# Kernel optimization log

Measured on AMD Instinct MI355X. Metric: run time of the kernel, lower is better.

Reference implementation:

```python
import jax, jax.numpy as jnp
import numpy as np

D_MODEL = 1024
NUM_HEADS = 16
HEAD_DIM = D_MODEL // NUM_HEADS
NEG_INF = -1e9


def setup_inputs() -> dict:
    key = jax.random.key(0)
    ks = jax.random.split(key, 9)
    B, S, SI = 4, 1024, 512
    scale = 1.0 / np.sqrt(D_MODEL)
    return {
        "hidden_states": jax.random.normal(ks[0], (B, S, D_MODEL), jnp.float32),
        "image_hidden_states": jax.random.normal(ks[1], (B, SI, D_MODEL), jnp.float32),
        "attention_mask": jax.random.randint(ks[2], (B, 1, S, S + SI), 0, 2, jnp.int32),
        "w_q": jax.random.normal(ks[3], (D_MODEL, D_MODEL), jnp.float32) * scale,
        "w_k": jax.random.normal(ks[4], (D_MODEL, D_MODEL), jnp.float32) * scale,
        "w_v": jax.random.normal(ks[5], (D_MODEL, D_MODEL), jnp.float32) * scale,
        "u_k": jax.random.normal(ks[6], (D_MODEL, D_MODEL), jnp.float32) * scale,
        "u_v": jax.random.normal(ks[7], (D_MODEL, D_MODEL), jnp.float32) * scale,
        "w_o": jax.random.normal(ks[8], (D_MODEL, D_MODEL), jnp.float32) * scale,
    }


def _split_heads(x):
    # [B, S, D] -> [B, H, S, Dh]
    B, S, _ = x.shape
    return x.reshape(B, S, NUM_HEADS, HEAD_DIM).transpose(0, 2, 1, 3)


def reference(hidden_states, image_hidden_states, attention_mask,
              w_q, w_k, w_v, u_k, u_v, w_o):
    # nn.Linear(bias=False): y = x @ W.T
    q = _split_heads(hidden_states @ w_q.T)          # [B,H,S,Dh]
    k = _split_heads(hidden_states @ w_k.T)          # [B,H,S,Dh]
    v = _split_heads(hidden_states @ w_v.T)
    k_img = _split_heads(image_hidden_states @ u_k.T)  # [B,H,SI,Dh]
    v_img = _split_heads(image_hidden_states @ u_v.T)
    k = jnp.concatenate([k, k_img], axis=2)          # [B,H,S+SI,Dh]
    v = jnp.concatenate([v, v_img], axis=2)

    scores = jnp.einsum('bhqd,bhkd->bhqk', q, k) / np.sqrt(HEAD_DIM)
    scores = jnp.where(attention_mask == 0, NEG_INF, scores)
    p_attn = jax.nn.softmax(scores, axis=-1)         # dropout p=0.0 (eval)
    x = jnp.einsum('bhqk,bhkd->bhqd', p_attn, v)     # [B,H,S,Dh]
    B, H, S, Dh = x.shape
    x = x.transpose(0, 2, 1, 3).reshape(B, S, D_MODEL)
    return x @ w_o.T
```

## Files before the change

### kernel.cpp

```cpp
#include <hip/hip_runtime.h>
#include <stdint.h>


typedef unsigned short u16;
typedef short bf16x8v __attribute__((ext_vector_type(8)));
typedef float f32x4 __attribute__((ext_vector_type(4)));

__device__ __forceinline__ u16 f2bf(float f) {
  union { float f; uint32_t u; } x; x.f = f;
  uint32_t r = x.u + 0x7FFFu + ((x.u >> 16) & 1u);
  return (u16)(r >> 16);
}

__device__ __forceinline__ uint32_t cvtpk(float a, float b) {
  uint32_t r;
  asm("v_cvt_pk_bf16_f32 %0, %1, %2" : "=v"(r) : "v"(a), "v"(b));
  return r;
}

__device__ __forceinline__ float maskand(float e, uint32_t msrc, int off) {
  uint32_t mm = (uint32_t)((int32_t)(msrc << (31 - off)) >> 31);
  union { float f; uint32_t u; } x; x.f = e; x.u &= mm; return x.f;
}

__device__ __forceinline__ void gl_lds16(const u16* g, u16* l) {
  __builtin_amdgcn_global_load_lds((const __attribute__((address_space(1))) unsigned int*)g,
                                   (__attribute__((address_space(3))) unsigned int*)l,
                                   16, 0, 0);
}

__global__ __launch_bounds__(256) void mask_pack(const int* __restrict__ mk,
                                                 uint32_t* __restrict__ Mw) {
  int w = blockIdx.x * 256 + threadIdx.x;
  const int4* p = (const int4*)(mk + (size_t)w * 32);
  uint32_t bits = 0;
  #pragma unroll
  for (int c = 0; c < 8; ++c) {
    int4 v = p[c];
    bits |= (uint32_t)(v.x != 0) << (4 * c);
    bits |= (uint32_t)(v.y != 0) << (4 * c + 1);
    bits |= (uint32_t)(v.z != 0) << (4 * c + 2);
    bits |= (uint32_t)(v.w != 0) << (4 * c + 3);
  }
  Mw[w] = bits;
}

__global__ __launch_bounds__(512, 2) void gemm_qkv(
    const float* __restrict__ Hs, const float* __restrict__ Im,
    const float* __restrict__ Wq, const float* __restrict__ Wk, const float* __restrict__ Wv,
    const float* __restrict__ Uk, const float* __restrict__ Uv,
    u16* __restrict__ Qd, u16* __restrict__ Kd, u16* __restrict__ Vd)
{
  __shared__ __align__(16) u16 As[2 * 16384];
  __shared__ __align__(16) u16 Bs[2 * 16384];
  const int hb = blockIdx.x;
  const int xcd = hb & 7, slot = hb >> 3;
  int bid = (slot < 24) ? xcd * 24 + slot : 192 + xcd * 8 + (slot - 24);
  const float *Ap, *Bp;
  int bm, bn, mode;
  if (bid < 192) { mode = 4; bm = (bid / 12) * 256; bn = (bid % 12) * 256;
                   Ap = Hs + (size_t)bm * 1024;
                   Bp = ((bn < 1024) ? Wq : (bn < 2048) ? Wk : Wv) + (size_t)(bn & 1023) * 1024; }
  else           { mode = 5; int r = bid - 192; bm = (r >> 3) * 256; bn = (r & 7) * 256;
                   Ap = Im + (size_t)bm * 1024;
                   Bp = ((bn < 1024) ? Uk : Uv) + (size_t)(bn & 1023) * 1024; }
  const int tid = threadIdx.x, lane = tid & 63, wave = tid >> 6;
  const int wr = wave >> 2, wc = wave & 3;
  const int g = lane >> 4, c = lane & 15, cs = c & 7;
  const int srow = tid >> 3;
  const int pch  = tid & 7;
  const int gsw  = (pch ^ (srow & 7)) * 8;

  f32x4 zf = {0.f, 0.f, 0.f, 0.f};
  f32x4 acc[8][4];
  #pragma unroll
  for (int f = 0; f < 8; ++f)
    #pragma unroll
    for (int nf = 0; nf < 4; ++nf) acc[f][nf] = zf;

  float4 sa[4][2], sb[4][2];

  #define LOAD_A(kt)                                                               \
    _Pragma("unroll")                                                              \
    for (int j_ = 0; j_ < 4; ++j_) {                                               \
      const float* p_ = Ap + (size_t)(j_ * 64 + srow) * 1024 + (kt) * 64 + gsw;    \
      sa[j_][0] = *(const float4*)p_;                                              \
      sa[j_][1] = *(const float4*)(p_ + 4);                                        \
    }
  #define LOAD_B(kt)                                                               \
    _Pragma("unroll")                                                              \
    for (int j_ = 0; j_ < 4; ++j_) {                                               \
      const float* p_ = Bp + (size_t)(j_ * 64 + srow) * 1024 + (kt) * 64 + gsw;    \
      sb[j_][0] = *(const float4*)p_;                                              \
      sb[j_][1] = *(const float4*)(p_ + 4);                                        \
    }
  #define CVT_A(buf)                                                               \
    _Pragma("unroll")                                                              \
    for (int j_ = 0; j_ < 4; ++j_) {                                               \
      uint4 w_;                                                                    \
      w_.x = cvtpk(sa[j_][0].x, sa[j_][0].y);                                      \
      w_.y = cvtpk(sa[j_][0].z, sa[j_][0].w);                                      \
      w_.z = cvtpk(sa[j_][1].x, sa[j_][1].y);                                      \
      w_.w = cvtpk(sa[j_][1].z, sa[j_][1].w);                                      \
      *(uint4*)&As[(buf) + (j_ * 64 + srow) * 64 + pch * 8] = w_;                  \
    }
  #define CVT_B(buf)                                                               \
    _Pragma("unroll")                                                              \
    for (int j_ = 0; j_ < 4; ++j_) {                                               \
      uint4 w_;                                                                    \
      w_.x = cvtpk(sb[j_][0].x, sb[j_][0].y);                                      \
      w_.y = cvtpk(sb[j_][0].z, sb[j_][0].w);                                      \
      w_.z = cvtpk(sb[j_][1].x, sb[j_][1].y);                                      \
      w_.w = cvtpk(sb[j_][1].z, sb[j_][1].w);                                      \
      *(uint4*)&Bs[(buf) + (j_ * 64 + srow) * 64 + pch * 8] = w_;                  \
    }

  LOAD_A(0); LOAD_B(0);
  CVT_A(0);  CVT_B(0);
  __syncthreads();

  for (int kt = 0; kt < 16; ++kt) {
    const int bc = (kt & 1) * 16384;
    const int bx = bc ^ 16384;
    if (kt < 15) LOAD_A(kt + 1);

    bf16x8v Bf[4][2];
    #pragma unroll
    for (int nf = 0; nf < 4; ++nf)
      #pragma unroll
      for (int ks = 0; ks < 2; ++ks)
        Bf[nf][ks] = *(const bf16x8v*)&Bs[bc + (wc * 64 + nf * 16 + c) * 64 + ((ks * 4 + g) ^ cs) * 8];

    #pragma unroll
    for (int p = 0; p < 4; ++p) {
      bf16x8v Af[2][2];
      #pragma unroll
      for (int i = 0; i < 2; ++i)
        #pragma unroll
        for (int ks = 0; ks < 2; ++ks)
          Af[i][ks] = *(const bf16x8v*)&As[bc + (wr * 128 + (p * 2 + i) * 16 + c) * 64 + ((ks * 4 + g) ^ cs) * 8];
      __builtin_amdgcn_s_setprio(1);
      #pragma unroll
      for (int i = 0; i < 2; ++i)
        #pragma unroll
        for (int nf = 0; nf < 4; ++nf)
          #pragma unroll
          for (int ks = 0; ks < 2; ++ks)
            acc[p * 2 + i][nf] =
              __builtin_amdgcn_mfma_f32_16x16x32_bf16(Af[i][ks], Bf[nf][ks], acc[p * 2 + i][nf], 0, 0, 0);
      __builtin_amdgcn_s_setprio(0);
      if (p == 1 && kt < 15) {
        __builtin_amdgcn_sched_barrier(0);
        CVT_A(bx);
        LOAD_B(kt + 1);
        __builtin_amdgcn_sched_barrier(0);
      }
    }
    if (kt < 15) {
      __builtin_amdgcn_sched_barrier(0);
      CVT_B(bx);
    }
    __syncthreads();
  }
  #undef LOAD_A
  #undef LOAD_B
  #undef CVT_A
  #undef CVT_B

  #pragma unroll
  for (int f = 0; f < 8; ++f) {
    #pragma unroll
    for (int nf = 0; nf < 4; ++nf) {
      #pragma unroll
      for (int j = 0; j < 4; ++j) {
        int gm = bm + wr * 128 + f * 16 + 4 * g + j;
        int gn = bn + wc * 64 + nf * 16 + c;
        float v = acc[f][nf][j];
        if (mode == 4) {
          int b_ = gm >> 10, s_ = gm & 1023;
          if (gn < 1024)      Qd[(size_t)gm * 1024 + gn] = f2bf(v * 0.18033688011112042f);
          else if (gn < 2048) Kd[(size_t)(b_ * 1536 + s_) * 1024 + (gn - 1024)] = f2bf(v);
          else                Vd[(size_t)(b_ * 1024 + (gn - 2048)) * 1536 + s_] = f2bf(v);
        } else {
          int b_ = gm >> 9, s_ = gm & 511;
          if (gn < 1024) Kd[(size_t)(b_ * 1536 + 1024 + s_) * 1024 + gn] = f2bf(v);
          else           Vd[(size_t)(b_ * 1024 + (gn - 1024)) * 1536 + 1024 + s_] = f2bf(v);
        }
      }
    }
  }
}

__global__ __launch_bounds__(256) void gemm_out(const u16* __restrict__ A, const float* __restrict__ Bw,
                                                float* __restrict__ Cout)
{
  __shared__ __align__(16) u16 As2[2 * 8192];
  __shared__ __align__(16) u16 Bs2[2 * 8192];
  const int hb = blockIdx.x;
  const int xcd = hb & 7, slot = hb >> 3;
  const int rg = xcd * 4 + (slot >> 3);
  const int cg = slot & 7;
  const int bm = rg * 128, bn = cg * 128;
  const int tid  = threadIdx.x;
  const int lane = tid & 63, wave = tid >> 6;
  const int wr = wave >> 1, wc = wave & 1;
  const int g = lane >> 4, c = lane & 15, cs = c & 7;
  const int sr  = tid >> 3;
  const int pch = tid & 7;
  const int gsw = (pch ^ (sr & 7)) * 8;

  f32x4 zf = {0.f, 0.f, 0.f, 0.f};
  f32x4 acc[4][4];
  #pragma unroll
  for (int mi = 0; mi < 4; ++mi)
    #pragma unroll
    for (int ni = 0; ni < 4; ++ni) acc[mi][ni] = zf;

  float4 sb[4][2];

  #define STG_A(buf, kt)                                                           \
    _Pragma("unroll")                                                              \
    for (int q_ = 0; q_ < 4; ++q_) {                                               \
      int row_ = q_ * 32 + sr;                                                     \
      gl_lds16(A + (size_t)(bm + row_) * 1024 + (kt) * 64 + gsw,                   \
               &As2[(buf) + row_ * 64 + pch * 8]);                                 \
    }
  #define LOAD_B(kt)                                                               \
    _Pragma("unroll")                                                              \
    for (int q_ = 0; q_ < 4; ++q_) {                                               \
      const float* p_ = Bw + (size_t)(bn + q_ * 32 + sr) * 1024 + (kt) * 64 + gsw; \
      sb[q_][0] = *(const float4*)p_;                                              \
      sb[q_][1] = *(const float4*)(p_ + 4);                                        \
    }
  #define CVT_B(buf)                                                               \
    _Pragma("unroll")                                                              \
    for (int q_ = 0; q_ < 4; ++q_) {                                               \
      uint4 w_;                                                                    \
      w_.x = cvtpk(sb[q_][0].x, sb[q_][0].y);                                      \
      w_.y = cvtpk(sb[q_][0].z, sb[q_][0].w);                                      \
      w_.z = cvtpk(sb[q_][1].x, sb[q_][1].y);                                      \
      w_.w = cvtpk(sb[q_][1].z, sb[q_][1].w);                                      \
      *(uint4*)&Bs2[(buf) + (q_ * 32 + sr) * 64 + pch * 8] = w_;                   \
    }

  STG_A(0, 0);
  LOAD_B(0);
  CVT_B(0);
  __syncthreads();

  for (int kt = 0; kt < 16; ++kt) {
    const int bc = (kt & 1) * 8192;
    const int bx = bc ^ 8192;
    if (kt < 15) { STG_A(bx, kt + 1); LOAD_B(kt + 1); }

    #pragma unroll
    for (int ks = 0; ks < 2; ++ks) {
      bf16x8v af[4], bfr[4];
      #pragma unroll
      for (int mi = 0; mi < 4; ++mi)
        af[mi] = *(const bf16x8v*)&As2[bc + (wr * 64 + mi * 16 + c) * 64 + ((ks * 4 + g) ^ cs) * 8];
      #pragma unroll
      for (int ni = 0; ni < 4; ++ni)
        bfr[ni] = *(const bf16x8v*)&Bs2[bc + (wc * 64 + ni * 16 + c) * 64 + ((ks * 4 + g) ^ cs) * 8];
      __builtin_amdgcn_s_setprio(1);
      #pragma unroll
      for (int mi = 0; mi < 4; ++mi)
        #pragma unroll
        for (int ni = 0; ni < 4; ++ni)
          acc[mi][ni] = __builtin_amdgcn_mfma_f32_16x16x32_bf16(af[mi], bfr[ni], acc[mi][ni], 0, 0, 0);
      __builtin_amdgcn_s_setprio(0);
    }
    if (kt < 15) {
      __builtin_amdgcn_sched_barrier(0);
      CVT_B(bx);
    }
    __syncthreads();
  }
  #undef STG_A
  #undef LOAD_B
  #undef CVT_B

  #pragma unroll
  for (int mi = 0; mi < 4; ++mi)
    #pragma unroll
    for (int ni = 0; ni < 4; ++ni)
      #pragma unroll
      for (int j = 0; j < 4; ++j) {
        int gm = bm + wr * 64 + mi * 16 + 4 * g + j;
        int gn = bn + wc * 64 + ni * 16 + c;
        Cout[(size_t)gm * 1024 + gn] = acc[mi][ni][j];
      }
}

__global__ __launch_bounds__(256) void attn_kernel(const u16* __restrict__ Q, const u16* __restrict__ Kc,
                                                   const u16* __restrict__ Vt,
                                                   const uint32_t* __restrict__ Mw,
                                                   u16* __restrict__ AO)
{
  const int bid = blockIdx.x;
  const int grp = bid & 63;
  const int qt  = bid >> 6;
  const int h = grp & 15, b = grp >> 4;
  const int q0 = qt * 64;
  const int tid = threadIdx.x, lane = tid & 63, wave = tid >> 6;
  const int g = lane >> 4, c = lane & 15;
  const int qw = q0 + wave * 16;

  __shared__ __align__(16) u16 Ks[64 * 64];
  __shared__ __align__(16) u16 Vs[64 * 64];
  __shared__ __align__(16) u16 Ps[4][16 * 72];

  bf16x8v qf0, qf1;
  {
    const u16* qp = Q + (size_t)(b * 1024 + qw + c) * 1024 + h * 64 + g * 8;
    qf0 = *(const bf16x8v*)qp;
    qf1 = *(const bf16x8v*)(qp + 32);
  }
  f32x4 zf = {0.f, 0.f, 0.f, 0.f};
  f32x4 O[4];
  float l = 0.f;
  #pragma unroll
  for (int dt = 0; dt < 4; ++dt) O[dt] = zf;

  const int sr  = tid >> 3;
  const int pch = tid & 7;
  const int swz = (pch ^ (sr & 7)) * 8;
  const int cs  = c & 7;
  const u16* Kbase = Kc + (size_t)(b * 1536) * 1024 + h * 64;
  const u16* Vbase = Vt + (size_t)(b * 1024 + h * 64) * 1536;
  const uint32_t* mrow = Mw + (size_t)(b * 1024 + qw + c) * 48;

  bf16x8v kr0, kr1, vr0, vr1;
  kr0 = *(const bf16x8v*)(Kbase + (size_t)sr * 1024 + pch * 8);
  kr1 = *(const bf16x8v*)(Kbase + (size_t)(32 + sr) * 1024 + pch * 8);
  vr0 = *(const bf16x8v*)(Vbase + (size_t)sr * 1536 + pch * 8);
  vr1 = *(const bf16x8v*)(Vbase + (size_t)(32 + sr) * 1536 + pch * 8);
  *(bf16x8v*)&Ks[sr * 64 + swz]        = kr0;
  *(bf16x8v*)&Ks[(32 + sr) * 64 + swz] = kr1;
  *(bf16x8v*)&Vs[sr * 64 + swz]        = vr0;
  *(bf16x8v*)&Vs[(32 + sr) * 64 + swz] = vr1;
  __syncthreads();

  for (int kt = 0; kt < 24; ++kt) {
    if (kt < 23) {
      const int ln = (kt + 1) * 64;
      kr0 = *(const bf16x8v*)(Kbase + (size_t)(ln + sr) * 1024 + pch * 8);
      kr1 = *(const bf16x8v*)(Kbase + (size_t)(ln + 32 + sr) * 1024 + pch * 8);
      vr0 = *(const bf16x8v*)(Vbase + (size_t)sr * 1536 + ln + pch * 8);
      vr1 = *(const bf16x8v*)(Vbase + (size_t)(32 + sr) * 1536 + ln + pch * 8);
    }
    uint2 mwv = *(const uint2*)(mrow + kt * 2);

    f32x4 s[4];
    __builtin_amdgcn_s_setprio(1);
    #pragma unroll
    for (int nt = 0; nt < 4; ++nt) {
      const u16* kr = &Ks[(nt * 16 + c) * 64];
      bf16x8v k0 = *(const bf16x8v*)&kr[(g ^ cs) * 8];
      bf16x8v k1 = *(const bf16x8v*)&kr[((4 + g) ^ cs) * 8];
      f32x4 z = zf;
      z = __builtin_amdgcn_mfma_f32_16x16x32_bf16(k0, qf0, z, 0, 0, 0);
      z = __builtin_amdgcn_mfma_f32_16x16x32_bf16(k1, qf1, z, 0, 0, 0);
      s[nt] = z;
    }
    __builtin_amdgcn_s_setprio(0);

    uint64_t mq = (((uint64_t)mwv.y << 32) | (uint64_t)mwv.x) >> (4 * g);
    uint32_t mlo = (uint32_t)mq, mhi = (uint32_t)(mq >> 32);
    #pragma unroll
    for (int nt = 0; nt < 4; ++nt) {
      uint32_t msrc = (nt < 2) ? mlo : mhi;
      #pragma unroll
      for (int j = 0; j < 4; ++j) {
        float e = exp2f(s[nt][j]);
        float p = maskand(e, msrc, 16 * (nt & 1) + j);
        s[nt][j] = p;
        l += p;
      }
    }

    u16* pw = &Ps[wave][0];
    #pragma unroll
    for (int nt = 0; nt < 4; ++nt) {
      uint2 pk2;
      pk2.x = cvtpk(s[nt][0], s[nt][1]);
      pk2.y = cvtpk(s[nt][2], s[nt][3]);
      *(uint2*)&pw[c * 72 + nt * 16 + g * 4] = pk2;
    }
    bf16x8v pb0 = *(const bf16x8v*)&pw[c * 72 + g * 8];
    bf16x8v pb1 = *(const bf16x8v*)&pw[c * 72 + 32 + g * 8];
    __builtin_amdgcn_s_setprio(1);
    #pragma unroll
    for (int dt = 0; dt < 4; ++dt) {
      const u16* vr = &Vs[(dt * 16 + c) * 64];
      bf16x8v v0 = *(const bf16x8v*)&vr[(g ^ cs) * 8];
      bf16x8v v1 = *(const bf16x8v*)&vr[((4 + g) ^ cs) * 8];
      O[dt] = __builtin_amdgcn_mfma_f32_16x16x32_bf16(v0, pb0, O[dt], 0, 0, 0);
      O[dt] = __builtin_amdgcn_mfma_f32_16x16x32_bf16(v1, pb1, O[dt], 0, 0, 0);
    }
    __builtin_amdgcn_s_setprio(0);

    __syncthreads();
    if (kt < 23) {
      *(bf16x8v*)&Ks[sr * 64 + swz]        = kr0;
      *(bf16x8v*)&Ks[(32 + sr) * 64 + swz] = kr1;
      *(bf16x8v*)&Vs[sr * 64 + swz]        = vr0;
      *(bf16x8v*)&Vs[(32 + sr) * 64 + swz] = vr1;
      __syncthreads();
    }
  }

  float r = l;
  r += __shfl_xor(r, 16);
  r += __shfl_xor(r, 32);
  float inv = 1.f / r;
  size_t ro = (size_t)(b * 1024 + qw + c) * 1024 + h * 64;
  #pragma unroll
  for (int dt = 0; dt < 4; ++dt) {
    uint2 st;
    st.x = cvtpk(O[dt][0] * inv, O[dt][1] * inv);
    st.y = cvtpk(O[dt][2] * inv, O[dt][3] * inv);
    *(uint2*)&AO[ro + dt * 16 + 4 * g] = st;
  }
}

extern "C" void kernel_launch(void* const* d_in, const int* in_sizes, int n_in,
                              void* d_out, int out_size, void* d_ws, size_t ws_size,
                              hipStream_t stream) {
  (void)in_sizes; (void)n_in; (void)out_size; (void)ws_size;
  const float* hs = (const float*)d_in[0];
  const float* im = (const float*)d_in[1];
  const int*   mk = (const int*)d_in[2];
  const float* wq = (const float*)d_in[3];
  const float* wk = (const float*)d_in[4];
  const float* wv = (const float*)d_in[5];
  const float* uk = (const float*)d_in[6];
  const float* uv = (const float*)d_in[7];
  const float* wo = (const float*)d_in[8];

  char* ws = (char*)d_ws;
  u16* Qb  = (u16*)(ws + 0);
  u16* Kb  = (u16*)(ws + 8388608);
  u16* Vtb = (u16*)(ws + 20971520);
  u16* AO  = (u16*)(ws + 33554432);
  uint32_t* Mw = (uint32_t*)(ws + 41943040);

  mask_pack<<<768, 256, 0, stream>>>(mk, Mw);
  gemm_qkv<<<256, 512, 0, stream>>>(hs, im, wq, wk, wv, uk, uv, Qb, Kb, Vtb);
  attn_kernel<<<1024, 256, 0, stream>>>(Qb, Kb, Vtb, Mw, AO);
  gemm_out<<<256, 256, 0, stream>>>(AO, wo, (float*)d_out);
}
```

Baseline: 158.9 us.

## Fuse mask bit-packing into QKV GEMM prologue and vectorize V-transpose stores

Removes the separate mask_pack launch and has each QKV GEMM thread pack mask words right after issuing its first tile loads. This saves one kernel launch and lets the mask read overlap with the GEMM's own loads. The epilogue is also split by output region so the branch on gn moves out of the inner loops, and the transposed V writes become packed 8-byte bf16 stores instead of scalar ones. The catch is that the GEMM prologue gets longer, since the ~25MB mask read now sits on the GEMM's critical path and may raise register pressure.

Result: faster. 133.7 us (-15.9%).

```diff
diff --git a/kernel.cpp b/kernel.cpp
--- a/kernel.cpp
+++ b/kernel.cpp
@@ -29,27 +29,13 @@
                                    16, 0, 0);
 }
 
-__global__ __launch_bounds__(256) void mask_pack(const int* __restrict__ mk,
-                                                 uint32_t* __restrict__ Mw) {
-  int w = blockIdx.x * 256 + threadIdx.x;
-  const int4* p = (const int4*)(mk + (size_t)w * 32);
-  uint32_t bits = 0;
-  #pragma unroll
-  for (int c = 0; c < 8; ++c) {
-    int4 v = p[c];
-    bits |= (uint32_t)(v.x != 0) << (4 * c);
-    bits |= (uint32_t)(v.y != 0) << (4 * c + 1);
-    bits |= (uint32_t)(v.z != 0) << (4 * c + 2);
-    bits |= (uint32_t)(v.w != 0) << (4 * c + 3);
-  }
-  Mw[w] = bits;
-}
-
 __global__ __launch_bounds__(512, 2) void gemm_qkv(
     const float* __restrict__ Hs, const float* __restrict__ Im,
     const float* __restrict__ Wq, const float* __restrict__ Wk, const float* __restrict__ Wv,
     const float* __restrict__ Uk, const float* __restrict__ Uv,
-    u16* __restrict__ Qd, u16* __restrict__ Kd, u16* __restrict__ Vd)
+    const int* __restrict__ Mk,
+    u16* __restrict__ Qd, u16* __restrict__ Kd, u16* __restrict__ Vd,
+    uint32_t* __restrict__ Mw)
 {
   __shared__ __align__(16) u16 As[2 * 16384];
   __shared__ __align__(16) u16 Bs[2 * 16384];
@@ -116,6 +102,37 @@
     }
 
   LOAD_A(0); LOAD_B(0);
+  {
+    const int fid = hb * 512 + tid;
+    #pragma unroll 1
+    for (int w = fid; w < 196608; w += 131072) {
+      const int4* p = (const int4*)(Mk + (size_t)w * 32);
+      uint32_t bits = 0;
+      #pragma unroll 1
+      for (int h_ = 0; h_ < 2; ++h_) {
+        int4 v0 = p[h_ * 4 + 0], v1 = p[h_ * 4 + 1];
+        int4 v2 = p[h_ * 4 + 2], v3 = p[h_ * 4 + 3];
+        int bo = h_ * 16;
+        bits |= (uint32_t)(v0.x != 0) << (bo + 0);
+        bits |= (uint32_t)(v0.y != 0) << (bo + 1);
+        bits |= (uint32_t)(v0.z != 0) << (bo + 2);
+        bits |= (uint32_t)(v0.w != 0) << (bo + 3);
+        bits |= (uint32_t)(v1.x != 0) << (bo + 4);
+        bits |= (uint32_t)(v1.y != 0) << (bo + 5);
+        bits |= (uint32_t)(v1.z != 0) << (bo + 6);
+        bits |= (uint32_t)(v1.w != 0) << (bo + 7);
+        bits |= (uint32_t)(v2.x != 0) << (bo + 8);
+        bits |= (uint32_t)(v2.y != 0) << (bo + 9);
+        bits |= (uint32_t)(v2.z != 0) << (bo + 10);
+        bits |= (uint32_t)(v2.w != 0) << (bo + 11);
+        bits |= (uint32_t)(v3.x != 0) << (bo + 12);
+        bits |= (uint32_t)(v3.y != 0) << (bo + 13);
+        bits |= (uint32_t)(v3.z != 0) << (bo + 14);
+        bits |= (uint32_t)(v3.w != 0) << (bo + 15);
+      }
+      Mw[w] = bits;
+    }
+  }
   CVT_A(0);  CVT_B(0);
   __syncthreads();
 
@@ -167,26 +184,71 @@
   #undef CVT_A
   #undef CVT_B
 
-  #pragma unroll
-  for (int f = 0; f < 8; ++f) {
-    #pragma unroll
-    for (int nf = 0; nf < 4; ++nf) {
-      #pragma unroll
-      for (int j = 0; j < 4; ++j) {
-        int gm = bm + wr * 128 + f * 16 + 4 * g + j;
-        int gn = bn + wc * 64 + nf * 16 + c;
-        float v = acc[f][nf][j];
-        if (mode == 4) {
+  const int gn0 = bn + wc * 64;
+  if (mode == 4) {
+    if (bn < 1024) {
+      #pragma unroll
+      for (int f = 0; f < 8; ++f)
+        #pragma unroll
+        for (int nf = 0; nf < 4; ++nf) {
+          int gm = bm + wr * 128 + f * 16 + 4 * g;
+          int gn = gn0 + nf * 16 + c;
+          #pragma unroll
+          for (int j = 0; j < 4; ++j)
+            Qd[(size_t)(gm + j) * 1024 + gn] = f2bf(acc[f][nf][j] * 0.18033688011112042f);
+        }
+    } else if (bn < 2048) {
+      #pragma unroll
+      for (int f = 0; f < 8; ++f)
+        #pragma unroll
+        for (int nf = 0; nf < 4; ++nf) {
+          int gm = bm + wr * 128 + f * 16 + 4 * g;
           int b_ = gm >> 10, s_ = gm & 1023;
-          if (gn < 1024)      Qd[(size_t)gm * 1024 + gn] = f2bf(v * 0.18033688011112042f);
-          else if (gn < 2048) Kd[(size_t)(b_ * 1536 + s_) * 1024 + (gn - 1024)] = f2bf(v);
-          else                Vd[(size_t)(b_ * 1024 + (gn - 2048)) * 1536 + s_] = f2bf(v);
-        } else {
+          int gn = gn0 - 1024 + nf * 16 + c;
+          #pragma unroll
+          for (int j = 0; j < 4; ++j)
+            Kd[(size_t)(b_ * 1536 + s_ + j) * 1024 + gn] = f2bf(acc[f][nf][j]);
+        }
+    } else {
+      #pragma unroll
+      for (int f = 0; f < 8; ++f)
+        #pragma unroll
+        for (int nf = 0; nf < 4; ++nf) {
+          int gm = bm + wr * 128 + f * 16 + 4 * g;
+          int b_ = gm >> 10, s_ = gm & 1023;
+          int d_ = gn0 - 2048 + nf * 16 + c;
+          uint2 st;
+          st.x = cvtpk(acc[f][nf][0], acc[f][nf][1]);
+          st.y = cvtpk(acc[f][nf][2], acc[f][nf][3]);
+          *(uint2*)&Vd[(size_t)(b_ * 1024 + d_) * 1536 + s_] = st;
+        }
+    }
+  } else {
+    if (bn < 1024) {
+      #pragma unroll
+      for (int f = 0; f < 8; ++f)
+        #pragma unroll
+        for (int nf = 0; nf < 4; ++nf) {
+          int gm = bm + wr * 128 + f * 16 + 4 * g;
           int b_ = gm >> 9, s_ = gm & 511;
-          if (gn < 1024) Kd[(size_t)(b_ * 1536 + 1024 + s_) * 1024 + gn] = f2bf(v);
-          else           Vd[(size_t)(b_ * 1024 + (gn - 1024)) * 1536 + 1024 + s_] = f2bf(v);
+          int gn = gn0 + nf * 16 + c;
+          #pragma unroll
+          for (int j = 0; j < 4; ++j)
+            Kd[(size_t)(b_ * 1536 + 1024 + s_ + j) * 1024 + gn] = f2bf(acc[f][nf][j]);
         }
-      }
+    } else {
+      #pragma unroll
+      for (int f = 0; f < 8; ++f)
+        #pragma unroll
+        for (int nf = 0; nf < 4; ++nf) {
+          int gm = bm + wr * 128 + f * 16 + 4 * g;
+          int b_ = gm >> 9, s_ = gm & 511;
+          int d_ = gn0 - 1024 + nf * 16 + c;
+          uint2 st;
+          st.x = cvtpk(acc[f][nf][0], acc[f][nf][1]);
+          st.y = cvtpk(acc[f][nf][2], acc[f][nf][3]);
+          *(uint2*)&Vd[(size_t)(b_ * 1024 + d_) * 1536 + 1024 + s_] = st;
+        }
     }
   }
 }
@@ -445,8 +507,7 @@
   u16* AO  = (u16*)(ws + 33554432);
   uint32_t* Mw = (uint32_t*)(ws + 41943040);
 
-  mask_pack<<<768, 256, 0, stream>>>(mk, Mw);
-  gemm_qkv<<<256, 512, 0, stream>>>(hs, im, wq, wk, wv, uk, uv, Qb, Kb, Vtb);
+  gemm_qkv<<<256, 512, 0, stream>>>(hs, im, wq, wk, wv, uk, uv, mk, Qb, Kb, Vtb, Mw);
   attn_kernel<<<1024, 256, 0, stream>>>(Qb, Kb, Vtb, Mw, AO);
   gemm_out<<<256, 256, 0, stream>>>(AO, wo, (float*)d_out);
 }
```
